# Kernel tuning notes

Hardware: AMD Instinct MI355X
Metric: run time of the kernel (lower is better)

The kernel has to match this reference:

```python
import jax, jax.numpy as jnp
import numpy as np

D_MODEL = 1024
N_HEADS = 16
D_HEAD = D_MODEL // N_HEADS          # 64
FRACTION_TO_ROTATE = 0.25
ROT_DIM = int(FRACTION_TO_ROTATE * D_HEAD)  # 16 (even)
ROPE_BASE = 10000.0


def setup_inputs() -> dict:
    key = jax.random.key(0)
    ks = jax.random.split(key, 10)
    B, S = 2, 2048
    init = lambda k, fan_in, shape: jax.random.normal(k, shape, jnp.float32) / np.sqrt(fan_in)
    return {
        "x": jax.random.normal(ks[0], (B, S, D_MODEL), jnp.float32),
        "Wq": init(ks[1], D_MODEL, (D_MODEL, D_MODEL)),
        "bq": jnp.zeros((D_MODEL,), jnp.float32),
        "Wk": init(ks[2], D_MODEL, (D_MODEL, D_MODEL)),
        "bk": jnp.zeros((D_MODEL,), jnp.float32),
        "Wv": init(ks[3], D_MODEL, (D_MODEL, D_MODEL)),
        "bv": jnp.zeros((D_MODEL,), jnp.float32),
        "Wo": init(ks[4], D_MODEL, (D_MODEL, D_MODEL)),
        "bo": jnp.zeros((D_MODEL,), jnp.float32),
    }


def _apply_partial_rope(t, cos, sin):
    # t: [B, H, S, d_head]; rotate first ROT_DIM dims, pass the rest through.
    rot, rest = t[..., :ROT_DIM], t[..., ROT_DIM:]
    half = ROT_DIM // 2
    t1, t2 = rot[..., :half], rot[..., half:]
    # cos/sin: [S, half] -> broadcast over [B, H]
    r1 = t1 * cos - t2 * sin
    r2 = t1 * sin + t2 * cos
    return jnp.concatenate([r1, r2, rest], axis=-1)


def reference(x, Wq, bq, Wk, bk, Wv, bv, Wo, bo):
    B, S, D = x.shape
    q = (x @ Wq + bq).reshape(B, S, N_HEADS, D_HEAD).transpose(0, 2, 1, 3)
    k = (x @ Wk + bk).reshape(B, S, N_HEADS, D_HEAD).transpose(0, 2, 1, 3)
    v = (x @ Wv + bv).reshape(B, S, N_HEADS, D_HEAD).transpose(0, 2, 1, 3)

    half = ROT_DIM // 2
    inv_freq = 1.0 / (ROPE_BASE ** (jnp.arange(half, dtype=jnp.float32) / half))
    angles = jnp.arange(S, dtype=jnp.float32)[:, None] * inv_freq  # [S, half]
    cos, sin = jnp.cos(angles), jnp.sin(angles)

    q = _apply_partial_rope(q, cos, sin)
    k = _apply_partial_rope(k, cos, sin)

    scale = 1.0 / np.sqrt(D_HEAD).astype(np.float32)
    scores = jnp.einsum("bhqd,bhkd->bhqk", q, k) * scale  # [B,H,S,S]
    causal = jnp.tril(jnp.ones((S, S), dtype=bool))
    scores = jnp.where(causal, scores, jnp.finfo(scores.dtype).min)
    probs = jax.nn.softmax(scores, axis=-1)

    out = jnp.einsum("bhqk,bhkd->bhqd", probs, v)  # [B,H,S,d_head]
    out = out.transpose(0, 2, 1, 3).reshape(B, S, D)
    return out @ Wo + bo
```

## Files before the change

kernel.cpp:

```cpp
#include <hip/hip_runtime.h>
#include <hip/hip_bf16.h>
#include <math.h>

constexpr int DM = 1024;
constexpr int SEQ = 2048;
constexpr int BATCH = 2;
constexpr int NH = 16;
constexpr int DH = 64;
constexpr int MROWS = BATCH * SEQ;
constexpr float SCALE = 0.125f;

typedef __attribute__((ext_vector_type(8))) short short8;
typedef __attribute__((ext_vector_type(4))) float f32x4;
typedef unsigned short ushort_t;

__device__ __forceinline__ unsigned short f2b(float f) {
    __hip_bfloat16 h = __float2bfloat16(f);
    return __builtin_bit_cast(unsigned short, h);
}
__device__ __forceinline__ float b2f(unsigned short u) {
    unsigned int t = ((unsigned int)u) << 16;
    return __builtin_bit_cast(float, t);
}
__device__ __forceinline__ unsigned int cvtpk_bf16(float lo, float hi) {
    unsigned int r;
    asm("v_cvt_pk_bf16_f32 %0, %1, %2" : "=v"(r) : "v"(lo), "v"(hi));
    return r;
}

__device__ __forceinline__ void gload16(const ushort_t* g, ushort_t* l) {
    __builtin_amdgcn_global_load_lds(
        (const __attribute__((address_space(1))) void*)g,
        (__attribute__((address_space(3))) void*)l, 16, 0, 0);
}

__global__ __launch_bounds__(256) void conv_x(const float* __restrict__ x,
                                              ushort_t* __restrict__ xb) {
    const size_t idx = (size_t)blockIdx.x * 256 + threadIdx.x;
    const float4* src = (const float4*)(x + idx * 8);
    float4 a = src[0], b = src[1];
    short8 v;
    v[0] = (short)f2b(a.x); v[1] = (short)f2b(a.y);
    v[2] = (short)f2b(a.z); v[3] = (short)f2b(a.w);
    v[4] = (short)f2b(b.x); v[5] = (short)f2b(b.y);
    v[6] = (short)f2b(b.z); v[7] = (short)f2b(b.w);
    *(short8*)(xb + idx * 8) = v;
}

__global__ __launch_bounds__(256) void conv_w(
    const float* __restrict__ Wq, const float* __restrict__ Wk,
    const float* __restrict__ Wv, const float* __restrict__ Wo,
    ushort_t* __restrict__ Wqt, ushort_t* __restrict__ Wkt,
    ushort_t* __restrict__ Wvt, ushort_t* __restrict__ Wot) {
    const float* W; ushort_t* Wt;
    switch (blockIdx.z) {
        case 0:  W = Wq; Wt = Wqt; break;
        case 1:  W = Wk; Wt = Wkt; break;
        case 2:  W = Wv; Wt = Wvt; break;
        default: W = Wo; Wt = Wot; break;
    }
    __shared__ float L[64][65];
    const int n0 = blockIdx.x * 64, k0 = blockIdx.y * 64;
    const int t = threadIdx.x;
    const int tr = t >> 4, tc4 = (t & 15) * 4;
#pragma unroll
    for (int i = 0; i < 4; ++i) {
        int kk = tr + i * 16;
        float4 v = *(const float4*)&W[(size_t)(k0 + kk) * DM + n0 + tc4];
        L[kk][tc4 + 0] = v.x; L[kk][tc4 + 1] = v.y;
        L[kk][tc4 + 2] = v.z; L[kk][tc4 + 3] = v.w;
    }
    __syncthreads();
#pragma unroll
    for (int i = 0; i < 4; ++i) {
        int nn = tr + i * 16;
        ushort4 u;
        u.x = f2b(L[tc4 + 0][nn]); u.y = f2b(L[tc4 + 1][nn]);
        u.z = f2b(L[tc4 + 2][nn]); u.w = f2b(L[tc4 + 3][nn]);
        *(ushort4*)&Wt[(size_t)(n0 + nn) * DM + k0 + tc4] = u;
    }
}

#define BM 128
#define BN 128
#define BKK 64

__device__ __forceinline__ void mfma_core(const ushort_t* __restrict__ A,
                                          const ushort_t* __restrict__ B,
                                          int row0, int col0,
                                          ushort_t* smem, f32x4 (&acc)[4][4]) {
    const int tid = threadIdx.x;
    const int wave = tid >> 6, lane = tid & 63;
    const int lg = lane >> 4, ln = lane & 15;
    const int wr = wave >> 1, wc = wave & 1;
    ushort_t* As = smem;
    ushort_t* Bs = smem + 8192;

    for (int kt = 0; kt < DM / BKK; ++kt) {
        __syncthreads();
#pragma unroll
        for (int i = 0; i < 4; ++i) {
            int f = i * 256 + tid;
            int r = f >> 3, p = f & 7, c = p ^ (r & 7);
            gload16(&A[(size_t)(row0 + r) * DM + kt * BKK + c * 8], &As[f * 8]);
            gload16(&B[(size_t)(col0 + r) * DM + kt * BKK + c * 8], &Bs[f * 8]);
        }
        __syncthreads();

        short8 af[4][2], bf[4][2];
#pragma unroll
        for (int mi = 0; mi < 4; ++mi) {
            int r = wr * 64 + mi * 16 + ln;
#pragma unroll
            for (int ks = 0; ks < 2; ++ks) {
                int c = ks * 4 + lg;
                af[mi][ks] = *(const short8*)&As[r * 64 + ((c ^ (r & 7)) * 8)];
            }
        }
#pragma unroll
        for (int ni = 0; ni < 4; ++ni) {
            int r = wc * 64 + ni * 16 + ln;
#pragma unroll
            for (int ks = 0; ks < 2; ++ks) {
                int c = ks * 4 + lg;
                bf[ni][ks] = *(const short8*)&Bs[r * 64 + ((c ^ (r & 7)) * 8)];
            }
        }
#pragma unroll
        for (int ks = 0; ks < 2; ++ks)
#pragma unroll
            for (int mi = 0; mi < 4; ++mi)
#pragma unroll
                for (int ni = 0; ni < 4; ++ni)
                    acc[mi][ni] = __builtin_amdgcn_mfma_f32_16x16x32_bf16(
                        af[mi][ks], bf[ni][ks], acc[mi][ni], 0, 0, 0);
    }
}

__global__ __launch_bounds__(256) void mfma_gemm_qkv(
    const ushort_t* __restrict__ xb,
    const ushort_t* __restrict__ Wqt, const ushort_t* __restrict__ Wkt,
    const ushort_t* __restrict__ Wvt,
    const float* __restrict__ bq, const float* __restrict__ bk,
    const float* __restrict__ bv,
    ushort_t* __restrict__ qb, ushort_t* __restrict__ kb,
    ushort_t* __restrict__ vtb) {
    const ushort_t* W; const float* bias;
    if (blockIdx.z == 0)      { W = Wqt; bias = bq; }
    else if (blockIdx.z == 1) { W = Wkt; bias = bk; }
    else                      { W = Wvt; bias = bv; }

    const int row0 = blockIdx.y * BM;
    const int col0 = blockIdx.x * BN;
    __shared__ ushort_t smem[16384];
    f32x4 acc[4][4] = {};
    mfma_core(xb, W, row0, col0, smem, acc);

    const int tid = threadIdx.x;
    const int wave = tid >> 6, lane = tid & 63;
    const int lg = lane >> 4, ln = lane & 15;
    const int wr = wave >> 1, wc = wave & 1;
    const bool isV = (blockIdx.z == 2);

    __syncthreads();
    ushort_t* Cs = smem;
#pragma unroll
    for (int mi = 0; mi < 4; ++mi)
#pragma unroll
        for (int ni = 0; ni < 4; ++ni)
#pragma unroll
            for (int r = 0; r < 4; ++r) {
                int mrel = wr * 64 + mi * 16 + lg * 4 + r;
                int nrel = wc * 64 + ni * 16 + ln;
                float v = acc[mi][ni][r] + bias[col0 + nrel];
                Cs[isV ? (nrel * 128 + mrel) : (mrel * 128 + nrel)] = f2b(v);
            }
    __syncthreads();

    if (!isV) {
        ushort_t* out = (blockIdx.z == 0) ? qb : kb;
#pragma unroll
        for (int i = 0; i < 8; ++i) {
            int f = i * 256 + tid;
            int rrow = f >> 4, c8 = f & 15;
            int m = row0 + rrow;
            int b = m >> 11, s = m & (SEQ - 1);
            int n = col0 + c8 * 8;
            int h = n >> 6, d = n & 63;
            short8 val;
            if (d < 16) {
                const ushort_t* base = &Cs[rrow * 128 + (c8 & 8) * 8];
                const bool hi = (d >= 8);
#pragma unroll
                for (int j = 0; j < 8; ++j) {
                    float t1 = b2f(base[j]);
                    float t2 = b2f(base[8 + j]);
                    float invf = __expf(-(float)j * 1.1512925465f);
                    float ang = (float)s * invf;
                    float c_, si_;
                    __sincosf(ang, &si_, &c_);
                    val[j] = (short)f2b(hi ? (t1 * si_ + t2 * c_)
                                           : (t1 * c_ - t2 * si_));
                }
            } else {
                val = *(const short8*)&Cs[rrow * 128 + c8 * 8];
            }
            *(short8*)&out[((size_t)((b * NH + h) * SEQ) + s) * DH + d] = val;
        }
    } else {
#pragma unroll
        for (int i = 0; i < 8; ++i) {
            int f = i * 256 + tid;
            int nrow = f >> 4, c8 = f & 15;
            int n = col0 + nrow;
            int h = n >> 6, d = n & 63;
            int m = row0 + c8 * 8;
            int b = m >> 11, s = m & (SEQ - 1);
            *(short8*)&vtb[((size_t)((b * NH + h) * DH) + d) * SEQ + s] =
                *(const short8*)&Cs[nrow * 128 + c8 * 8];
        }
    }
}

__global__ __launch_bounds__(256) void mfma_gemm_out(
    const ushort_t* __restrict__ ctxb, const ushort_t* __restrict__ Wot,
    const float* __restrict__ bo, float* __restrict__ out) {
    const int row0 = blockIdx.y * BM;
    const int col0 = blockIdx.x * BN;
    __shared__ ushort_t smem[16384];
    f32x4 acc[4][4] = {};
    mfma_core(ctxb, Wot, row0, col0, smem, acc);

    const int tid = threadIdx.x;
    const int wave = tid >> 6, lane = tid & 63;
    const int lg = lane >> 4, ln = lane & 15;
    const int wr = wave >> 1, wc = wave & 1;
#pragma unroll
    for (int mi = 0; mi < 4; ++mi)
#pragma unroll
        for (int ni = 0; ni < 4; ++ni)
#pragma unroll
            for (int r = 0; r < 4; ++r) {
                int m = row0 + wr * 64 + mi * 16 + lg * 4 + r;
                int n = col0 + wc * 64 + ni * 16 + ln;
                out[(size_t)m * DM + n] = acc[mi][ni][r] + bo[n];
            }
}

#define AQT 64
#define AKT 64
#define NQT (SEQ / AQT)

__global__ __launch_bounds__(256) void attn_mfma(
    const ushort_t* __restrict__ qb, const ushort_t* __restrict__ kb,
    const ushort_t* __restrict__ vtb, ushort_t* __restrict__ ctxb) {
    constexpr float C1 = 0.18033688f;
    constexpr float THR2 = 11.5415603f;
    const int bh = blockIdx.x;
    const int y = blockIdx.y;
    const int y0 = y & 7, g = y >> 3;
    const int qt = (g == 0) ? y0 : (g == 1) ? (15 - y0)
                 : (g == 2) ? (16 + y0) : (31 - y0);
    const int q0 = qt * AQT;

    const int tid = threadIdx.x;
    const int wave = tid >> 6;
    const int lane = tid & 63;
    const int lg = lane >> 4;
    const int ln = lane & 15;

    __shared__ ushort_t KT[2][64 * 64];
    __shared__ ushort_t VT[2][64 * 64];
    __shared__ ushort_t PT[4][16 * 64];

    const ushort_t* kbase = kb + (size_t)bh * SEQ * DH;
    const ushort_t* vbase = vtb + (size_t)bh * DH * SEQ;
    const int b = bh >> 4, h = bh & 15;

    const ushort_t* qrow = qb + ((size_t)bh * SEQ + q0 + wave * 16 + ln) * DH;
    short8 qf0 = *(const short8*)&qrow[lg * 8];
    short8 qf1 = *(const short8*)&qrow[32 + lg * 8];

    f32x4 o[4];
#pragma unroll
    for (int nt = 0; nt < 4; nt++) o[nt] = f32x4{0.f, 0.f, 0.f, 0.f};
    float m2 = -1e30f, l = 0.f;

    const int ntiles = qt + 1;

#pragma unroll
    for (int i = 0; i < 2; i++) {
        int f = i * 256 + tid;
        int r = f >> 3, p = f & 7, c = p ^ (r & 7);
        gload16(&kbase[(size_t)r * DH + c * 8], &KT[0][f * 8]);
        gload16(&vbase[(size_t)r * SEQ + c * 8], &VT[0][f * 8]);
    }

    int cur = 0;
    for (int t = 0; t < ntiles; ++t) {
        __syncthreads();

        if (t + 1 < ntiles) {
            const int nb0 = (t + 1) * AKT;
            const int nxt = cur ^ 1;
#pragma unroll
            for (int i = 0; i < 2; i++) {
                int f = i * 256 + tid;
                int r = f >> 3, p = f & 7, c = p ^ (r & 7);
                gload16(&kbase[(size_t)(nb0 + r) * DH + c * 8], &KT[nxt][f * 8]);
                gload16(&vbase[(size_t)r * SEQ + nb0 + c * 8], &VT[nxt][f * 8]);
            }
        }

        float st[4][4];
        __builtin_amdgcn_s_setprio(1);
#pragma unroll
        for (int kt = 0; kt < 4; kt++) {
            f32x4 acc = f32x4{0.f, 0.f, 0.f, 0.f};
            int krow = kt * 16 + ln;
            short8 b0 = *(const short8*)&KT[cur][krow * 64 + ((lg ^ (krow & 7)) * 8)];
            short8 b1 = *(const short8*)&KT[cur][krow * 64 + (((4 + lg) ^ (krow & 7)) * 8)];
            acc = __builtin_amdgcn_mfma_f32_16x16x32_bf16(b0, qf0, acc, 0, 0, 0);
            acc = __builtin_amdgcn_mfma_f32_16x16x32_bf16(b1, qf1, acc, 0, 0, 0);
#pragma unroll
            for (int r = 0; r < 4; r++) st[kt][r] = acc[r];
        }
        __builtin_amdgcn_s_setprio(0);

        if (t == ntiles - 1) {
            const int qrel = wave * 16 + ln;
#pragma unroll
            for (int kt = 0; kt < 4; kt++)
#pragma unroll
                for (int r = 0; r < 4; r++)
                    if (kt * 16 + lg * 4 + r > qrel) st[kt][r] = -1e30f;
        }

        float smax = st[0][0];
#pragma unroll
        for (int kt = 0; kt < 4; kt++)
#pragma unroll
            for (int r = 0; r < 4; r++) smax = fmaxf(smax, st[kt][r]);
        smax = fmaxf(smax, __shfl_xor(smax, 16));
        smax = fmaxf(smax, __shfl_xor(smax, 32));
        const float m2c = C1 * smax;

        if (!__all(m2c <= m2 + THR2)) {
            float m2n = fmaxf(m2, m2c);
            float corr = exp2f(m2 - m2n);
            m2 = m2n;
            l *= corr;
#pragma unroll
            for (int r = 0; r < 4; r++) {
                float c_o = __shfl(corr, (lane & 48) | (lg * 4 + r));
#pragma unroll
                for (int nt = 0; nt < 4; nt++) o[nt][r] *= c_o;
            }
        }

        float lsum = 0.f;
#pragma unroll
        for (int kt = 0; kt < 4; kt++) {
            float pv[4];
#pragma unroll
            for (int r = 0; r < 4; r++) {
                pv[r] = exp2f(fmaf(C1, st[kt][r], -m2));
                lsum += pv[r];
            }
            uint2 pk;
            pk.x = cvtpk_bf16(pv[0], pv[1]);
            pk.y = cvtpk_bf16(pv[2], pv[3]);
            int addr = ln * 64 + (((kt * 2 + (lg >> 1)) ^ (ln & 7)) * 8) + (lg & 1) * 4;
            *(uint2*)&PT[wave][addr] = pk;
        }
        lsum += __shfl_xor(lsum, 16);
        lsum += __shfl_xor(lsum, 32);
        l += lsum;

        short8 pa0 = *(const short8*)&PT[wave][ln * 64 + ((lg ^ (ln & 7)) * 8)];
        short8 pa1 = *(const short8*)&PT[wave][ln * 64 + (((4 + lg) ^ (ln & 7)) * 8)];
        __builtin_amdgcn_s_setprio(1);
#pragma unroll
        for (int nt = 0; nt < 4; nt++) {
            int vrow = nt * 16 + ln;
            short8 vb0 = *(const short8*)&VT[cur][vrow * 64 + ((lg ^ (vrow & 7)) * 8)];
            short8 vb1 = *(const short8*)&VT[cur][vrow * 64 + (((4 + lg) ^ (vrow & 7)) * 8)];
            o[nt] = __builtin_amdgcn_mfma_f32_16x16x32_bf16(pa0, vb0, o[nt], 0, 0, 0);
            o[nt] = __builtin_amdgcn_mfma_f32_16x16x32_bf16(pa1, vb1, o[nt], 0, 0, 0);
        }
        __builtin_amdgcn_s_setprio(0);

        cur ^= 1;
    }

    const float rcp = 1.f / l;
#pragma unroll
    for (int r = 0; r < 4; r++) {
        float invl = __shfl(rcp, (lane & 48) | (lg * 4 + r));
        int qg = q0 + wave * 16 + lg * 4 + r;
        ushort_t* op = ctxb + ((size_t)(b * SEQ + qg)) * DM + h * DH;
#pragma unroll
        for (int nt = 0; nt < 4; nt++)
            op[nt * 16 + ln] = f2b(o[nt][r] * invl);
    }
}

extern "C" void kernel_launch(void* const* d_in, const int* in_sizes, int n_in,
                              void* d_out, int out_size, void* d_ws, size_t ws_size,
                              hipStream_t stream) {
    const float* x  = (const float*)d_in[0];
    const float* Wq = (const float*)d_in[1];
    const float* bq = (const float*)d_in[2];
    const float* Wk = (const float*)d_in[3];
    const float* bk = (const float*)d_in[4];
    const float* Wv = (const float*)d_in[5];
    const float* bv = (const float*)d_in[6];
    const float* Wo = (const float*)d_in[7];
    const float* bo = (const float*)d_in[8];
    float* out = (float*)d_out;

    constexpr size_t TSZ = (size_t)MROWS * DM;
    constexpr size_t WSZ = (size_t)DM * DM;
    ushort_t* xb  = (ushort_t*)d_ws;
    ushort_t* Wqt = xb + TSZ;
    ushort_t* Wkt = Wqt + WSZ;
    ushort_t* Wvt = Wkt + WSZ;
    ushort_t* Wot = Wvt + WSZ;
    ushort_t* qbp = Wot + WSZ;
    ushort_t* kbp = qbp + TSZ;
    ushort_t* vtp = kbp + TSZ;
    ushort_t* ctxb = vtp + TSZ;

    conv_x<<<TSZ / 8 / 256, 256, 0, stream>>>(x, xb);
    conv_w<<<dim3(16, 16, 4), 256, 0, stream>>>(Wq, Wk, Wv, Wo, Wqt, Wkt, Wvt, Wot);

    mfma_gemm_qkv<<<dim3(DM / BN, MROWS / BM, 3), 256, 0, stream>>>(
        xb, Wqt, Wkt, Wvt, bq, bk, bv, qbp, kbp, vtp);

    attn_mfma<<<dim3(BATCH * NH, NQT), 256, 0, stream>>>(qbp, kbp, vtp, ctxb);

    mfma_gemm_out<<<dim3(DM / BN, MROWS / BM), 256, 0, stream>>>(ctxb, Wot, bo, out);
}
```

Baseline: 137.6 us.

## Double-buffer GEMM shared-memory tiles with BK 32 and prefetch next tile

Reworks the GEMM main loop to double-buffer LDS. The K tile shrinks from 64 to 32 so two buffers fit in the same shared memory, and the next tile's global-to-LDS load is issued before the current tile's MFMAs. This cuts one barrier per iteration and overlaps load latency with compute. It also raises wave priority around the MFMA block. The trade-off is twice as many loop iterations with less MFMA work each, so barrier and loop overhead per unit of compute goes up.

```diff
diff --git a/kernel.cpp b/kernel.cpp
--- a/kernel.cpp
+++ b/kernel.cpp
@@ -83,7 +83,21 @@
 
 #define BM 128
 #define BN 128
-#define BKK 64
+#define BKK 32
+#define NKT (DM / BKK)
+
+__device__ __forceinline__ void stage_tile(const ushort_t* __restrict__ A,
+                                           const ushort_t* __restrict__ B,
+                                           int row0, int col0, int kt,
+                                           ushort_t* As, ushort_t* Bs, int tid) {
+#pragma unroll
+    for (int i = 0; i < 2; ++i) {
+        int f = i * 256 + tid;
+        int r = f >> 2, c = (f & 3) ^ (r & 3);
+        gload16(&A[(size_t)(row0 + r) * DM + kt * BKK + c * 8], &As[f * 8]);
+        gload16(&B[(size_t)(col0 + r) * DM + kt * BKK + c * 8], &Bs[f * 8]);
+    }
+}
 
 __device__ __forceinline__ void mfma_core(const ushort_t* __restrict__ A,
                                           const ushort_t* __restrict__ B,
@@ -93,47 +107,41 @@
     const int wave = tid >> 6, lane = tid & 63;
     const int lg = lane >> 4, ln = lane & 15;
     const int wr = wave >> 1, wc = wave & 1;
-    ushort_t* As = smem;
-    ushort_t* Bs = smem + 8192;
-
-    for (int kt = 0; kt < DM / BKK; ++kt) {
-        __syncthreads();
-#pragma unroll
-        for (int i = 0; i < 4; ++i) {
-            int f = i * 256 + tid;
-            int r = f >> 3, p = f & 7, c = p ^ (r & 7);
-            gload16(&A[(size_t)(row0 + r) * DM + kt * BKK + c * 8], &As[f * 8]);
-            gload16(&B[(size_t)(col0 + r) * DM + kt * BKK + c * 8], &Bs[f * 8]);
-        }
-        __syncthreads();
-
-        short8 af[4][2], bf[4][2];
+
+    stage_tile(A, B, row0, col0, 0, smem, smem + 4096, tid);
+    __syncthreads();
+
+    int cur = 0;
+    for (int kt = 0; kt < NKT; ++kt) {
+        ushort_t* As = smem + cur * 8192;
+        ushort_t* Bs = As + 4096;
+        if (kt + 1 < NKT) {
+            ushort_t* An = smem + (cur ^ 1) * 8192;
+            stage_tile(A, B, row0, col0, kt + 1, An, An + 4096, tid);
+        }
+
+        short8 af[4], bf[4];
 #pragma unroll
         for (int mi = 0; mi < 4; ++mi) {
             int r = wr * 64 + mi * 16 + ln;
-#pragma unroll
-            for (int ks = 0; ks < 2; ++ks) {
-                int c = ks * 4 + lg;
-                af[mi][ks] = *(const short8*)&As[r * 64 + ((c ^ (r & 7)) * 8)];
-            }
+            af[mi] = *(const short8*)&As[r * 32 + ((lg ^ (r & 3)) * 8)];
         }
 #pragma unroll
         for (int ni = 0; ni < 4; ++ni) {
             int r = wc * 64 + ni * 16 + ln;
-#pragma unroll
-            for (int ks = 0; ks < 2; ++ks) {
-                int c = ks * 4 + lg;
-                bf[ni][ks] = *(const short8*)&Bs[r * 64 + ((c ^ (r & 7)) * 8)];
-            }
-        }
-#pragma unroll
-        for (int ks = 0; ks < 2; ++ks)
-#pragma unroll
-            for (int mi = 0; mi < 4; ++mi)
-#pragma unroll
-                for (int ni = 0; ni < 4; ++ni)
-                    acc[mi][ni] = __builtin_amdgcn_mfma_f32_16x16x32_bf16(
-                        af[mi][ks], bf[ni][ks], acc[mi][ni], 0, 0, 0);
+            bf[ni] = *(const short8*)&Bs[r * 32 + ((lg ^ (r & 3)) * 8)];
+        }
+        __builtin_amdgcn_s_setprio(1);
+#pragma unroll
+        for (int mi = 0; mi < 4; ++mi)
+#pragma unroll
+            for (int ni = 0; ni < 4; ++ni)
+                acc[mi][ni] = __builtin_amdgcn_mfma_f32_16x16x32_bf16(
+                    af[mi], bf[ni], acc[mi][ni], 0, 0, 0);
+        __builtin_amdgcn_s_setprio(0);
+
+        __syncthreads();
+        cur ^= 1;
     }
 }
 
```

Measured after the change: 123.9 us. 9.9% less time.
